# Kernel tuning notes

Measured on AMD Instinct MI355X. Metric: run time of the kernel, lower is better.

Reference implementation:

```python
import jax, jax.numpy as jnp
import numpy as np

N, E, B = 50000, 800000, 512
D_IN = 128
H = [128, 128, 128, 256, 128]
OUT = 2


def setup_inputs() -> dict:
    key = jax.random.key(0)
    ks = jax.random.split(key, 24)

    def w(k, i, o):
        return (jax.random.normal(k, (i, o), jnp.float32) / np.sqrt(i)).astype(jnp.float32)

    x = jax.random.normal(ks[0], (N, D_IN), jnp.float32)
    edge_index = jax.random.randint(ks[1], (2, E), 0, N)
    batch = (jnp.arange(N) * B) // N  # sorted graph ids, every graph non-empty

    return {
        "x": x,
        "edge_index": edge_index,
        "batch": batch,
        # SAGEConv k: out = mean_aggr(x_j) @ Wl + bl + x @ Wr  (PyG default: bias on lin_l, none on lin_r)
        "Wl1": w(ks[2], D_IN, H[0]), "Wr1": w(ks[3], D_IN, H[0]), "bl1": jnp.zeros((H[0],), jnp.float32),
        "Wl2": w(ks[4], H[0], H[1]), "Wr2": w(ks[5], H[0], H[1]), "bl2": jnp.zeros((H[1],), jnp.float32),
        "Wl3": w(ks[6], H[1], H[2]), "Wr3": w(ks[7], H[1], H[2]), "bl3": jnp.zeros((H[2],), jnp.float32),
        "W_f1": w(ks[8], H[2], H[3]), "b_f1": jnp.zeros((H[3],), jnp.float32),
        "W_f2": w(ks[9], H[3], H[4]), "b_f2": jnp.zeros((H[4],), jnp.float32),
        "W_sm": w(ks[10], H[4], OUT), "b_sm": jnp.zeros((OUT,), jnp.float32),
        "W_news": w(ks[11], D_IN, OUT), "b_news": jnp.zeros((OUT,), jnp.float32),
        "W_cat": w(ks[12], 2 * OUT, 1), "b_cat": jnp.zeros((1,), jnp.float32),
    }


def _sage(x, src, dst, Wl, Wr, bl):
    # mean aggregation of source-node features onto destination nodes
    msg = x[src]                                                     # [E, d] gather
    s = jax.ops.segment_sum(msg, dst, num_segments=N)                # [N, d] scatter-add
    cnt = jax.ops.segment_sum(jnp.ones((src.shape[0],), x.dtype), dst, num_segments=N)
    mean = s / jnp.maximum(cnt, 1.0)[:, None]
    return mean @ Wl + bl + x @ Wr


def reference(x, edge_index, batch, Wl1, Wr1, bl1, Wl2, Wr2, bl2, Wl3, Wr3, bl3,
              W_f1, b_f1, W_f2, b_f2, W_sm, b_sm, W_news, b_news, W_cat, b_cat):
    src, dst = edge_index[0], edge_index[1]
    h = jax.nn.relu(_sage(x, src, dst, Wl1, Wr1, bl1))
    h = jax.nn.relu(_sage(h, src, dst, Wl2, Wr2, bl2))
    h = jax.nn.relu(_sage(h, src, dst, Wl3, Wr3, bl3))

    h = jax.ops.segment_max(h, batch, num_segments=B)                # global_max_pool -> [B, H2]
    h = jax.nn.relu(h @ W_f1 + b_f1)
    h = jax.nn.relu(h @ W_f2 + b_f2)
    h = jax.nn.relu(h @ W_sm + b_sm)                                 # [B, OUT]

    # root = first node index of each graph (batch is sorted)
    root = jax.ops.segment_min(jnp.arange(N), batch, num_segments=B)  # [B]
    news = jax.nn.relu(x[root] @ W_news + b_news)                    # [B, OUT]

    out = jnp.concatenate([h, news], axis=-1) @ W_cat + b_cat        # [B, 1]
    return jax.nn.sigmoid(out)
```

## Files before the change

kernel.cpp:

```cpp
#include <hip/hip_runtime.h>
#include <hip/hip_bf16.h>
#include <math.h>

#define D 128
#define SA 144

typedef __attribute__((ext_vector_type(8))) short bf16x8;
typedef __attribute__((ext_vector_type(4))) float f32x4;

static __device__ __forceinline__ short f2b(float f) {
    unsigned u = __builtin_bit_cast(unsigned, f);
    unsigned r = (u + 0x7FFFu + ((u >> 16) & 1u)) >> 16;
    return (short)r;
}
static __device__ __forceinline__ float b2f(short b) {
    unsigned u = ((unsigned)(unsigned short)b) << 16;
    return __builtin_bit_cast(float, u);
}


__global__ __launch_bounds__(256) void conv_x_kernel(const float* __restrict__ x,
                                                     short* __restrict__ xb, int total4) {
    int idx = blockIdx.x * 256 + threadIdx.x;
    if (idx >= total4) return;
    float4 v = ((const float4*)x)[idx];
    short4 o;
    o.x = f2b(v.x); o.y = f2b(v.y); o.z = f2b(v.z); o.w = f2b(v.w);
    ((short4*)xb)[idx] = o;
}

struct WPack { const float* w[6]; short* o[6]; };
__global__ __launch_bounds__(256) void conv_w_kernel(WPack p) {
    const float* W = p.w[blockIdx.y];
    short* O = p.o[blockIdx.y];
    int idx = blockIdx.x * 256 + threadIdx.x;
    int k = idx >> 7, nn = idx & 127;
    O[nn * D + k] = f2b(W[k * D + nn]);
}


__global__ void deg_kernel(const int* __restrict__ dst, int* __restrict__ deg, int E) {
    int e = blockIdx.x * blockDim.x + threadIdx.x;
    if (e < E) atomicAdd(&deg[dst[e]], 1);
}

__global__ __launch_bounds__(256) void block_sum_kernel(const int* __restrict__ deg,
                                                        int* __restrict__ bsum, int n) {
    __shared__ int red[256];
    int b = blockIdx.x, tid = threadIdx.x;
    int base = b * 1024 + tid * 4;
    int s = 0;
    if (base + 3 < n) {
        int4 v = *(const int4*)(deg + base);
        s = v.x + v.y + v.z + v.w;
    } else {
        for (int i = 0; i < 4; ++i) if (base + i < n) s += deg[base + i];
    }
    red[tid] = s;
    __syncthreads();
    for (int off = 128; off; off >>= 1) {
        if (tid < off) red[tid] += red[tid + off];
        __syncthreads();
    }
    if (tid == 0) bsum[b] = red[0];
}

__global__ void bsum_scan_kernel(int* __restrict__ bsum, int nb) {
    int lane = threadIdx.x;
    int v = (lane < nb) ? bsum[lane] : 0;
    for (int off = 1; off < 64; off <<= 1) {
        int t = __shfl_up(v, off, 64);
        if (lane >= off) v += t;
    }
    int ex = __shfl_up(v, 1, 64);
    if (lane == 0) ex = 0;
    if (lane < nb) bsum[lane] = ex;
}

__global__ __launch_bounds__(256) void emit_kernel(const int* __restrict__ deg,
                                                   const int* __restrict__ boff,
                                                   int* __restrict__ row_ptr,
                                                   float* __restrict__ inv_deg,
                                                   int* __restrict__ gcursor,
                                                   int n, int E) {
    __shared__ int tsum[256];
    int b = blockIdx.x, tid = threadIdx.x;
    int base = b * 1024 + tid * 4;
    int v[4]; int s = 0;
#pragma unroll
    for (int i = 0; i < 4; ++i) {
        int idx = base + i;
        v[i] = (idx < n) ? deg[idx] : 0;
        s += v[i];
    }
    tsum[tid] = s;
    __syncthreads();
    for (int off = 1; off < 256; off <<= 1) {
        int t = (tid >= off) ? tsum[tid - off] : 0;
        __syncthreads();
        tsum[tid] += t;
        __syncthreads();
    }
    int run = boff[b] + tsum[tid] - s;
#pragma unroll
    for (int i = 0; i < 4; ++i) {
        int idx = base + i;
        if (idx < n) {
            row_ptr[idx] = run;
            inv_deg[idx] = 1.0f / (float)((v[i] > 0) ? v[i] : 1);
            if ((idx & 127) == 0) gcursor[idx >> 7] = run;
            run += v[i];
        }
    }
    if (b == 0 && tid == 0) row_ptr[n] = E;
}


#define EPB 4096
__global__ __launch_bounds__(256) void bin_kernel(const int* __restrict__ src,
                                                  const int* __restrict__ dst,
                                                  int* __restrict__ gcursor,
                                                  int2* __restrict__ binned, int E) {
    __shared__ int hist[512];
    __shared__ int base[512];
    int tid = threadIdx.x;
    int e0 = blockIdx.x * EPB;
    hist[tid] = 0; hist[tid + 256] = 0;
    __syncthreads();
    int sv[16], dv[16], bv[16];
#pragma unroll
    for (int i = 0; i < 16; ++i) {
        int e = e0 + i * 256 + tid;
        if (e < E) {
            sv[i] = src[e]; dv[i] = dst[e];
            bv[i] = dv[i] >> 7;
            atomicAdd(&hist[bv[i]], 1);
        } else bv[i] = -1;
    }
    __syncthreads();
    {
        int c0 = hist[tid];
        base[tid] = c0 ? atomicAdd(&gcursor[tid], c0) : 0;
        hist[tid] = 0;
        int c1 = hist[tid + 256];
        base[tid + 256] = c1 ? atomicAdd(&gcursor[tid + 256], c1) : 0;
        hist[tid + 256] = 0;
    }
    __syncthreads();
#pragma unroll
    for (int i = 0; i < 16; ++i) {
        if (bv[i] >= 0) {
            int off = atomicAdd(&hist[bv[i]], 1);
            binned[base[bv[i]] + off] = make_int2(sv[i], dv[i]);
        }
    }
}

__global__ __launch_bounds__(256) void place_kernel(const int2* __restrict__ binned,
                                                    const int* __restrict__ row_ptr,
                                                    int* __restrict__ col, int n) {
    __shared__ int cur[128];
    int b = blockIdx.x, tid = threadIdx.x;
    int node0 = b << 7;
    if (tid < 128) {
        int nd = node0 + tid;
        cur[tid] = (nd < n) ? row_ptr[nd] : 0;
    }
    int node1 = node0 + 128; if (node1 > n) node1 = n;
    int start = row_ptr[node0];
    int end   = row_ptr[node1];
    __syncthreads();
    for (int i = start + tid; i < end; i += 256) {
        int2 e = binned[i];
        int pos = atomicAdd(&cur[e.y & 127], 1);
        col[pos] = e.x;
    }
}


__global__ void agg_kernel(const short* __restrict__ h, const int* __restrict__ row_ptr,
                           const int* __restrict__ col, const float* __restrict__ inv_deg,
                           short* __restrict__ out, int n) {
    int w = (blockIdx.x * blockDim.x + threadIdx.x) >> 6;
    int lane = threadIdx.x & 63;
    if (w >= n) return;
    int s = row_ptr[w], e = row_ptr[w + 1];
    int g = lane >> 4, l16 = lane & 15;
    float acc[8];
#pragma unroll
    for (int q = 0; q < 8; ++q) acc[q] = 0.f;
    for (int p = s + g; p < e; p += 4) {
        int j = col[p];
        bf16x8 v = *(const bf16x8*)(h + (size_t)j * D + l16 * 8);
#pragma unroll
        for (int q = 0; q < 8; ++q) acc[q] += b2f(v[q]);
    }
#pragma unroll
    for (int q = 0; q < 8; ++q) {
        acc[q] += __shfl_xor(acc[q], 16, 64);
        acc[q] += __shfl_xor(acc[q], 32, 64);
    }
    if (g == 0) {
        float sc = inv_deg[w];
        bf16x8 o;
#pragma unroll
        for (int q = 0; q < 8; ++q) o[q] = f2b(acc[q] * sc);
        *(bf16x8*)(out + (size_t)w * D + l16 * 8) = o;
    }
}


__global__ __launch_bounds__(256) void sage_mm_mfma(
        const short* __restrict__ Aagg, const short* __restrict__ Hin,
        const short* __restrict__ WlT,  const short* __restrict__ WrT,
        const float* __restrict__ bl,   short* __restrict__ out, int M) {
    __shared__ short lA[128 * SA];
    __shared__ short lW[128 * SA];
    int tid  = threadIdx.x;
    int wave = tid >> 6, lane = tid & 63;
    int row0 = blockIdx.x * 128;
    int mrow = wave * 32;
    int m16  = lane & 15, quad = lane >> 4;

    f32x4 acc[2][8];
#pragma unroll
    for (int i = 0; i < 2; ++i)
#pragma unroll
        for (int j = 0; j < 8; ++j) acc[i][j] = (f32x4){0.f, 0.f, 0.f, 0.f};

#pragma unroll
    for (int half = 0; half < 2; ++half) {
        const short* A = half ? Hin : Aagg;
        const short* W = half ? WrT : WlT;
#pragma unroll
        for (int it = 0; it < 8; ++it) {
            int idx = it * 256 + tid;
            int r = idx >> 4, c8 = (idx & 15) << 3;
            bf16x8 va = {0, 0, 0, 0, 0, 0, 0, 0};
            int gr = row0 + r;
            if (gr < M) va = *(const bf16x8*)(A + (size_t)gr * D + c8);
            *(bf16x8*)(&lA[r * SA + c8]) = va;
            bf16x8 vw = *(const bf16x8*)(W + r * D + c8);
            *(bf16x8*)(&lW[r * SA + c8]) = vw;
        }
        __syncthreads();
#pragma unroll
        for (int ks = 0; ks < 4; ++ks) {
            int kb = ks * 32 + quad * 8;
            bf16x8 a0 = *(const bf16x8*)(&lA[(mrow +      m16) * SA + kb]);
            bf16x8 a1 = *(const bf16x8*)(&lA[(mrow + 16 + m16) * SA + kb]);
#pragma unroll
            for (int nt = 0; nt < 8; ++nt) {
                bf16x8 b = *(const bf16x8*)(&lW[(nt * 16 + m16) * SA + kb]);
                acc[0][nt] = __builtin_amdgcn_mfma_f32_16x16x32_bf16(a0, b, acc[0][nt], 0, 0, 0);
                acc[1][nt] = __builtin_amdgcn_mfma_f32_16x16x32_bf16(a1, b, acc[1][nt], 0, 0, 0);
            }
        }
        __syncthreads();
    }
#pragma unroll
    for (int mt = 0; mt < 2; ++mt) {
#pragma unroll
        for (int r = 0; r < 4; ++r) {
            int grow = row0 + mrow + mt * 16 + quad * 4 + r;
            if (grow < M) {
#pragma unroll
                for (int nt = 0; nt < 8; ++nt) {
                    int gcol = nt * 16 + m16;
                    float v = acc[mt][nt][r] + bl[gcol];
                    out[(size_t)grow * D + gcol] = f2b(fmaxf(v, 0.f));
                }
            }
        }
    }
}


__global__ void pool_kernel(const short* __restrict__ h, const int* __restrict__ batch,
                            float* __restrict__ pooled, int* __restrict__ root, int n) {
    int g = blockIdx.x;
    int f = threadIdx.x;
    int lo = 0, hi = n;
    while (lo < hi) { int m = (lo + hi) >> 1; if (batch[m] < g) lo = m + 1; else hi = m; }
    int start = lo;
    hi = n;
    while (lo < hi) { int m = (lo + hi) >> 1; if (batch[m] < g + 1) lo = m + 1; else hi = m; }
    int end = lo;
    if (f == 0) root[g] = start;
    float m = -3.4e38f;
    for (int i = start; i < end; ++i) m = fmaxf(m, b2f(h[(size_t)i * D + f]));
    pooled[(size_t)g * D + f] = m;
}


__global__ __launch_bounds__(256) void head_kernel(
        const float* __restrict__ pooled, const int* __restrict__ root,
        const float* __restrict__ x,
        const float* __restrict__ W_f1, const float* __restrict__ b_f1,
        const float* __restrict__ W_f2, const float* __restrict__ b_f2,
        const float* __restrict__ W_sm, const float* __restrict__ b_sm,
        const float* __restrict__ W_news, const float* __restrict__ b_news,
        const float* __restrict__ W_cat, const float* __restrict__ b_cat,
        float* __restrict__ out) {
    int g = blockIdx.x;
    int tid = threadIdx.x;
    __shared__ float p[128], t1[256], t2[128], hs[2], nw[2];
    if (tid < 128) p[tid] = pooled[(size_t)g * D + tid];
    __syncthreads();
    float a1 = b_f1[tid];
    for (int k = 0; k < 128; ++k) a1 += p[k] * W_f1[k * 256 + tid];
    t1[tid] = fmaxf(a1, 0.f);
    __syncthreads();
    if (tid < 128) {
        float a2 = b_f2[tid];
        for (int k = 0; k < 256; ++k) a2 += t1[k] * W_f2[k * 128 + tid];
        t2[tid] = fmaxf(a2, 0.f);
    }
    __syncthreads();
    if (tid < 2) {
        float a3 = b_sm[tid];
        for (int k = 0; k < 128; ++k) a3 += t2[k] * W_sm[k * 2 + tid];
        hs[tid] = fmaxf(a3, 0.f);
        const float* xr = x + (size_t)root[g] * D;
        float a4 = b_news[tid];
        for (int k = 0; k < 128; ++k) a4 += xr[k] * W_news[k * 2 + tid];
        nw[tid] = fmaxf(a4, 0.f);
    }
    __syncthreads();
    if (tid == 0) {
        float o = b_cat[0] + hs[0] * W_cat[0] + hs[1] * W_cat[1]
                           + nw[0] * W_cat[2] + nw[1] * W_cat[3];
        out[g] = 1.0f / (1.0f + __expf(-o));
    }
}


extern "C" void kernel_launch(void* const* d_in, const int* in_sizes, int n_in,
                              void* d_out, int out_size, void* d_ws, size_t ws_size,
                              hipStream_t stream) {
    const float* x      = (const float*)d_in[0];
    const int*   edge   = (const int*)d_in[1];
    const int*   batch  = (const int*)d_in[2];
    const float* Wl1 = (const float*)d_in[3];
    const float* Wr1 = (const float*)d_in[4];
    const float* bl1 = (const float*)d_in[5];
    const float* Wl2 = (const float*)d_in[6];
    const float* Wr2 = (const float*)d_in[7];
    const float* bl2 = (const float*)d_in[8];
    const float* Wl3 = (const float*)d_in[9];
    const float* Wr3 = (const float*)d_in[10];
    const float* bl3 = (const float*)d_in[11];
    const float* W_f1 = (const float*)d_in[12];
    const float* b_f1 = (const float*)d_in[13];
    const float* W_f2 = (const float*)d_in[14];
    const float* b_f2 = (const float*)d_in[15];
    const float* W_sm = (const float*)d_in[16];
    const float* b_sm = (const float*)d_in[17];
    const float* W_news = (const float*)d_in[18];
    const float* b_news = (const float*)d_in[19];
    const float* W_cat = (const float*)d_in[20];
    const float* b_cat = (const float*)d_in[21];
    float* out = (float*)d_out;

    const int E = in_sizes[1] / 2;
    const int n = in_sizes[2];
    const int B = out_size;

    const int* src = edge;
    const int* dst = edge + E;

    char* ws = (char*)d_ws;
    size_t off = 0;
    auto carve = [&](size_t bytes) {
        void* pt = ws + off;
        off = (off + bytes + 255) & ~(size_t)255;
        return pt;
    };
    int*   deg     = (int*)carve((size_t)n * 4);
    int*   row_ptr = (int*)carve((size_t)(n + 1) * 4);
    float* inv_deg = (float*)carve((size_t)n * 4);
    int*   col     = (int*)carve((size_t)E * 4);
    int*   bsum    = (int*)carve((size_t)256 * 4);
    int*   gcursor = (int*)carve((size_t)512 * 4);
    int2*  binned  = (int2*)carve((size_t)E * 8);
    short* xb      = (short*)carve((size_t)n * D * 2);
    short* aggb    = (short*)carve((size_t)n * D * 2);
    short* hA      = (short*)carve((size_t)n * D * 2);
    short* hB      = (short*)carve((size_t)n * D * 2);
    short* Wt[6];
    for (int i = 0; i < 6; ++i) Wt[i] = (short*)carve((size_t)D * D * 2);
    float* pooled  = (float*)carve((size_t)B * D * 4);
    int*   root    = (int*)carve((size_t)B * 4);
    (void)ws_size;

    int total4 = n * D / 4;
    conv_x_kernel<<<(total4 + 255) / 256, 256, 0, stream>>>(x, xb, total4);
    WPack wp;
    wp.w[0] = Wl1; wp.w[1] = Wr1; wp.w[2] = Wl2; wp.w[3] = Wr2; wp.w[4] = Wl3; wp.w[5] = Wr3;
    for (int i = 0; i < 6; ++i) wp.o[i] = Wt[i];
    conv_w_kernel<<<dim3(64, 6), 256, 0, stream>>>(wp);

    int nb = (n + 1023) / 1024;
    int NB = (n + 127) / 128;
    hipMemsetAsync(deg, 0, (size_t)n * 4, stream);
    deg_kernel<<<(E + 255) / 256, 256, 0, stream>>>(dst, deg, E);
    block_sum_kernel<<<nb, 256, 0, stream>>>(deg, bsum, n);
    bsum_scan_kernel<<<1, 64, 0, stream>>>(bsum, nb);
    emit_kernel<<<nb, 256, 0, stream>>>(deg, bsum, row_ptr, inv_deg, gcursor, n, E);
    bin_kernel<<<(E + EPB - 1) / EPB, 256, 0, stream>>>(src, dst, gcursor, binned, E);
    place_kernel<<<NB, 256, 0, stream>>>(binned, row_ptr, col, n);

    int agg_blocks = (n * 64 + 255) / 256;
    int mm_blocks  = (n + 127) / 128;

    agg_kernel<<<agg_blocks, 256, 0, stream>>>(xb, row_ptr, col, inv_deg, aggb, n);
    sage_mm_mfma<<<mm_blocks, 256, 0, stream>>>(aggb, xb, Wt[0], Wt[1], bl1, hA, n);
    agg_kernel<<<agg_blocks, 256, 0, stream>>>(hA, row_ptr, col, inv_deg, aggb, n);
    sage_mm_mfma<<<mm_blocks, 256, 0, stream>>>(aggb, hA, Wt[2], Wt[3], bl2, hB, n);
    agg_kernel<<<agg_blocks, 256, 0, stream>>>(hB, row_ptr, col, inv_deg, aggb, n);
    sage_mm_mfma<<<mm_blocks, 256, 0, stream>>>(aggb, hB, Wt[4], Wt[5], bl3, hA, n);

    pool_kernel<<<B, 128, 0, stream>>>(hA, batch, pooled, root, n);
    head_kernel<<<B, 256, 0, stream>>>(pooled, root, x,
                                       W_f1, b_f1, W_f2, b_f2, W_sm, b_sm,
                                       W_news, b_news, W_cat, b_cat, out);
}
```

Baseline: 373.0 us.

## Fuse preprocessing and pool/head kernels, rebuild CSR from bucket histograms

Merges the x and weight bf16 conversions with a per-bucket destination histogram into one prep kernel. The per-node degree atomics and three-kernel scan are replaced by a 512-entry bucket scan, with per-node degrees and row pointers now computed inside place_kernel. The aggregation loop is unrolled by two to keep more gathers in flight, and pool and head are fused into a single kernel. The goal is fewer launches and fewer global atomics, at the cost of an extra pass over binned edges in place_kernel.

```diff
diff --git a/kernel.cpp b/kernel.cpp
--- a/kernel.cpp
+++ b/kernel.cpp
@@ -19,100 +19,73 @@
 }
 
 
-__global__ __launch_bounds__(256) void conv_x_kernel(const float* __restrict__ x,
-                                                     short* __restrict__ xb, int total4) {
-    int idx = blockIdx.x * 256 + threadIdx.x;
-    if (idx >= total4) return;
-    float4 v = ((const float4*)x)[idx];
-    short4 o;
-    o.x = f2b(v.x); o.y = f2b(v.y); o.z = f2b(v.z); o.w = f2b(v.w);
-    ((short4*)xb)[idx] = o;
-}
-
-struct WPack { const float* w[6]; short* o[6]; };
-__global__ __launch_bounds__(256) void conv_w_kernel(WPack p) {
-    const float* W = p.w[blockIdx.y];
-    short* O = p.o[blockIdx.y];
-    int idx = blockIdx.x * 256 + threadIdx.x;
-    int k = idx >> 7, nn = idx & 127;
-    O[nn * D + k] = f2b(W[k * D + nn]);
-}
-
-
-__global__ void deg_kernel(const int* __restrict__ dst, int* __restrict__ deg, int E) {
-    int e = blockIdx.x * blockDim.x + threadIdx.x;
-    if (e < E) atomicAdd(&deg[dst[e]], 1);
-}
-
-__global__ __launch_bounds__(256) void block_sum_kernel(const int* __restrict__ deg,
-                                                        int* __restrict__ bsum, int n) {
-    __shared__ int red[256];
-    int b = blockIdx.x, tid = threadIdx.x;
-    int base = b * 1024 + tid * 4;
-    int s = 0;
-    if (base + 3 < n) {
-        int4 v = *(const int4*)(deg + base);
-        s = v.x + v.y + v.z + v.w;
-    } else {
-        for (int i = 0; i < 4; ++i) if (base + i < n) s += deg[base + i];
-    }
-    red[tid] = s;
-    __syncthreads();
-    for (int off = 128; off; off >>= 1) {
-        if (tid < off) red[tid] += red[tid + off];
-        __syncthreads();
-    }
-    if (tid == 0) bsum[b] = red[0];
-}
-
-__global__ void bsum_scan_kernel(int* __restrict__ bsum, int nb) {
-    int lane = threadIdx.x;
-    int v = (lane < nb) ? bsum[lane] : 0;
-    for (int off = 1; off < 64; off <<= 1) {
-        int t = __shfl_up(v, off, 64);
-        if (lane >= off) v += t;
-    }
-    int ex = __shfl_up(v, 1, 64);
-    if (lane == 0) ex = 0;
-    if (lane < nb) bsum[lane] = ex;
-}
-
-__global__ __launch_bounds__(256) void emit_kernel(const int* __restrict__ deg,
-                                                   const int* __restrict__ boff,
-                                                   int* __restrict__ row_ptr,
-                                                   float* __restrict__ inv_deg,
-                                                   int* __restrict__ gcursor,
-                                                   int n, int E) {
-    __shared__ int tsum[256];
-    int b = blockIdx.x, tid = threadIdx.x;
-    int base = b * 1024 + tid * 4;
-    int v[4]; int s = 0;
-#pragma unroll
-    for (int i = 0; i < 4; ++i) {
-        int idx = base + i;
-        v[i] = (idx < n) ? deg[idx] : 0;
-        s += v[i];
-    }
-    tsum[tid] = s;
+struct PrepArgs {
+    const float* x; short* xb; int total4; int xb_blocks;
+    const float* w[6]; short* wo[6]; int w_blocks;
+    const int* dst; int* bcnt; int E;
+};
+
+__global__ __launch_bounds__(256) void prep_kernel(PrepArgs a) {
+    int bid = blockIdx.x, tid = threadIdx.x;
+    if (bid < a.xb_blocks) {
+        int idx = bid * 256 + tid;
+        if (idx < a.total4) {
+            float4 v = ((const float4*)a.x)[idx];
+            short4 o;
+            o.x = f2b(v.x); o.y = f2b(v.y); o.z = f2b(v.z); o.w = f2b(v.w);
+            ((short4*)a.xb)[idx] = o;
+        }
+        return;
+    }
+    if (bid < a.xb_blocks + a.w_blocks) {
+        int idx4 = (bid - a.xb_blocks) * 256 + tid;
+        int base = idx4 * 4;
+        int m = base >> 14;
+        int i = base & 16383;
+        const float* W = a.w[m];
+        short* O = a.wo[m];
+        int k = i >> 7, nn = i & 127;
+        float4 v = *(const float4*)(W + k * D + nn);
+        O[(nn + 0) * D + k] = f2b(v.x);
+        O[(nn + 1) * D + k] = f2b(v.y);
+        O[(nn + 2) * D + k] = f2b(v.z);
+        O[(nn + 3) * D + k] = f2b(v.w);
+        return;
+    }
+    __shared__ int hist[512];
+    hist[tid] = 0; hist[tid + 256] = 0;
+    __syncthreads();
+    int e0 = (bid - a.xb_blocks - a.w_blocks) * 4096;
+#pragma unroll
+    for (int i = 0; i < 16; ++i) {
+        int e = e0 + i * 256 + tid;
+        if (e < a.E) atomicAdd(&hist[a.dst[e] >> 7], 1);
+    }
+    __syncthreads();
+    int c = hist[tid];       if (c) atomicAdd(&a.bcnt[tid], c);
+    c = hist[tid + 256];     if (c) atomicAdd(&a.bcnt[tid + 256], c);
+}
+
+
+__global__ __launch_bounds__(256) void scan512_kernel(const int* __restrict__ bcnt,
+                                                      int* __restrict__ gbase,
+                                                      int* __restrict__ gcursor) {
+    __shared__ int sc[256];
+    int tid = threadIdx.x;
+    int a0 = bcnt[2 * tid], a1 = bcnt[2 * tid + 1];
+    int s = a0 + a1;
+    sc[tid] = s;
     __syncthreads();
     for (int off = 1; off < 256; off <<= 1) {
-        int t = (tid >= off) ? tsum[tid - off] : 0;
-        __syncthreads();
-        tsum[tid] += t;
-        __syncthreads();
-    }
-    int run = boff[b] + tsum[tid] - s;
-#pragma unroll
-    for (int i = 0; i < 4; ++i) {
-        int idx = base + i;
-        if (idx < n) {
-            row_ptr[idx] = run;
-            inv_deg[idx] = 1.0f / (float)((v[i] > 0) ? v[i] : 1);
-            if ((idx & 127) == 0) gcursor[idx >> 7] = run;
-            run += v[i];
-        }
-    }
-    if (b == 0 && tid == 0) row_ptr[n] = E;
+        int t = (tid >= off) ? sc[tid - off] : 0;
+        __syncthreads();
+        sc[tid] += t;
+        __syncthreads();
+    }
+    int ex = sc[tid] - s;
+    gbase[2 * tid] = ex;         gcursor[2 * tid] = ex;
+    gbase[2 * tid + 1] = ex + a0; gcursor[2 * tid + 1] = ex + a0;
+    if (tid == 255) gbase[512] = sc[255];
 }
 
 
@@ -156,19 +129,44 @@
     }
 }
 
+
 __global__ __launch_bounds__(256) void place_kernel(const int2* __restrict__ binned,
-                                                    const int* __restrict__ row_ptr,
-                                                    int* __restrict__ col, int n) {
+                                                    const int* __restrict__ gbase,
+                                                    int* __restrict__ row_ptr,
+                                                    float* __restrict__ inv_deg,
+                                                    int* __restrict__ col,
+                                                    int n, int E, int NB) {
+    __shared__ int cnt[128];
+    __shared__ int sc[128];
     __shared__ int cur[128];
     int b = blockIdx.x, tid = threadIdx.x;
     int node0 = b << 7;
+    int node1 = node0 + 128; if (node1 > n) node1 = n;
+    int start = gbase[b], end = gbase[b + 1];
+    if (tid < 128) cnt[tid] = 0;
+    __syncthreads();
+    for (int i = start + tid; i < end; i += 256)
+        atomicAdd(&cnt[binned[i].y & 127], 1);
+    __syncthreads();
+    if (tid < 128) sc[tid] = cnt[tid];
+    __syncthreads();
+    for (int off = 1; off < 128; off <<= 1) {
+        int t = (tid < 128 && tid >= off) ? sc[tid - off] : 0;
+        __syncthreads();
+        if (tid < 128) sc[tid] += t;
+        __syncthreads();
+    }
     if (tid < 128) {
         int nd = node0 + tid;
-        cur[tid] = (nd < n) ? row_ptr[nd] : 0;
-    }
-    int node1 = node0 + 128; if (node1 > n) node1 = n;
-    int start = row_ptr[node0];
-    int end   = row_ptr[node1];
+        if (nd < node1) {
+            int c = cnt[tid];
+            int base = start + sc[tid] - c;
+            row_ptr[nd] = base;
+            inv_deg[nd] = 1.0f / (float)((c > 0) ? c : 1);
+            cur[tid] = base;
+        }
+    }
+    if (b == NB - 1 && tid == 0) row_ptr[n] = E;
     __syncthreads();
     for (int i = start + tid; i < end; i += 256) {
         int2 e = binned[i];
@@ -189,7 +187,18 @@
     float acc[8];
 #pragma unroll
     for (int q = 0; q < 8; ++q) acc[q] = 0.f;
-    for (int p = s + g; p < e; p += 4) {
+    int p = s + g;
+    for (; p + 4 < e; p += 8) {
+        int j0 = col[p];
+        int j1 = col[p + 4];
+        bf16x8 v0 = *(const bf16x8*)(h + (size_t)j0 * D + l16 * 8);
+        bf16x8 v1 = *(const bf16x8*)(h + (size_t)j1 * D + l16 * 8);
+#pragma unroll
+        for (int q = 0; q < 8; ++q) acc[q] += b2f(v0[q]);
+#pragma unroll
+        for (int q = 0; q < 8; ++q) acc[q] += b2f(v1[q]);
+    }
+    if (p < e) {
         int j = col[p];
         bf16x8 v = *(const bf16x8*)(h + (size_t)j * D + l16 * 8);
 #pragma unroll
@@ -276,36 +285,31 @@
 }
 
 
-__global__ void pool_kernel(const short* __restrict__ h, const int* __restrict__ batch,
-                            float* __restrict__ pooled, int* __restrict__ root, int n) {
+__global__ __launch_bounds__(256) void poolhead_kernel(
+        const short* __restrict__ h, const int* __restrict__ batch,
+        const float* __restrict__ x,
+        const float* __restrict__ W_f1, const float* __restrict__ b_f1,
+        const float* __restrict__ W_f2, const float* __restrict__ b_f2,
+        const float* __restrict__ W_sm, const float* __restrict__ b_sm,
+        const float* __restrict__ W_news, const float* __restrict__ b_news,
+        const float* __restrict__ W_cat, const float* __restrict__ b_cat,
+        float* __restrict__ out, int n) {
     int g = blockIdx.x;
-    int f = threadIdx.x;
+    int tid = threadIdx.x;
+    int f = tid & 127, half = tid >> 7;
+    __shared__ float pm[256];
+    __shared__ float p[128], t1[256], t2[128], hs[2], nw[2];
     int lo = 0, hi = n;
     while (lo < hi) { int m = (lo + hi) >> 1; if (batch[m] < g) lo = m + 1; else hi = m; }
     int start = lo;
     hi = n;
     while (lo < hi) { int m = (lo + hi) >> 1; if (batch[m] < g + 1) lo = m + 1; else hi = m; }
     int end = lo;
-    if (f == 0) root[g] = start;
     float m = -3.4e38f;
-    for (int i = start; i < end; ++i) m = fmaxf(m, b2f(h[(size_t)i * D + f]));
-    pooled[(size_t)g * D + f] = m;
-}
-
-
-__global__ __launch_bounds__(256) void head_kernel(
-        const float* __restrict__ pooled, const int* __restrict__ root,
-        const float* __restrict__ x,
-        const float* __restrict__ W_f1, const float* __restrict__ b_f1,
-        const float* __restrict__ W_f2, const float* __restrict__ b_f2,
-        const float* __restrict__ W_sm, const float* __restrict__ b_sm,
-        const float* __restrict__ W_news, const float* __restrict__ b_news,
-        const float* __restrict__ W_cat, const float* __restrict__ b_cat,
-        float* __restrict__ out) {
-    int g = blockIdx.x;
-    int tid = threadIdx.x;
-    __shared__ float p[128], t1[256], t2[128], hs[2], nw[2];
-    if (tid < 128) p[tid] = pooled[(size_t)g * D + tid];
+    for (int i = start + half; i < end; i += 2) m = fmaxf(m, b2f(h[(size_t)i * D + f]));
+    pm[tid] = m;
+    __syncthreads();
+    if (tid < 128) p[tid] = fmaxf(pm[tid], pm[tid + 128]);
     __syncthreads();
     float a1 = b_f1[tid];
     for (int k = 0; k < 128; ++k) a1 += p[k] * W_f1[k * 256 + tid];
@@ -321,7 +325,7 @@
         float a3 = b_sm[tid];
         for (int k = 0; k < 128; ++k) a3 += t2[k] * W_sm[k * 2 + tid];
         hs[tid] = fmaxf(a3, 0.f);
-        const float* xr = x + (size_t)root[g] * D;
+        const float* xr = x + (size_t)start * D;
         float a4 = b_news[tid];
         for (int k = 0; k < 128; ++k) a4 += xr[k] * W_news[k * 2 + tid];
         nw[tid] = fmaxf(a4, 0.f);
@@ -376,11 +380,11 @@
         off = (off + bytes + 255) & ~(size_t)255;
         return pt;
     };
-    int*   deg     = (int*)carve((size_t)n * 4);
     int*   row_ptr = (int*)carve((size_t)(n + 1) * 4);
     float* inv_deg = (float*)carve((size_t)n * 4);
     int*   col     = (int*)carve((size_t)E * 4);
-    int*   bsum    = (int*)carve((size_t)256 * 4);
+    int*   bcnt    = (int*)carve((size_t)512 * 4);
+    int*   gbase   = (int*)carve((size_t)513 * 4);
     int*   gcursor = (int*)carve((size_t)512 * 4);
     int2*  binned  = (int2*)carve((size_t)E * 8);
     short* xb      = (short*)carve((size_t)n * D * 2);
@@ -389,26 +393,23 @@
     short* hB      = (short*)carve((size_t)n * D * 2);
     short* Wt[6];
     for (int i = 0; i < 6; ++i) Wt[i] = (short*)carve((size_t)D * D * 2);
-    float* pooled  = (float*)carve((size_t)B * D * 4);
-    int*   root    = (int*)carve((size_t)B * 4);
     (void)ws_size;
 
-    int total4 = n * D / 4;
-    conv_x_kernel<<<(total4 + 255) / 256, 256, 0, stream>>>(x, xb, total4);
-    WPack wp;
-    wp.w[0] = Wl1; wp.w[1] = Wr1; wp.w[2] = Wl2; wp.w[3] = Wr2; wp.w[4] = Wl3; wp.w[5] = Wr3;
-    for (int i = 0; i < 6; ++i) wp.o[i] = Wt[i];
-    conv_w_kernel<<<dim3(64, 6), 256, 0, stream>>>(wp);
-
-    int nb = (n + 1023) / 1024;
+    hipMemsetAsync(bcnt, 0, 512 * 4, stream);
+    PrepArgs pa;
+    pa.x = x; pa.xb = xb; pa.total4 = n * D / 4;
+    pa.xb_blocks = (pa.total4 + 255) / 256;
+    pa.w[0] = Wl1; pa.w[1] = Wr1; pa.w[2] = Wl2; pa.w[3] = Wr2; pa.w[4] = Wl3; pa.w[5] = Wr3;
+    for (int i = 0; i < 6; ++i) pa.wo[i] = Wt[i];
+    pa.w_blocks = (6 * D * D) / 1024;
+    pa.dst = dst; pa.bcnt = bcnt; pa.E = E;
+    int h_blocks = (E + 4095) / 4096;
+    prep_kernel<<<pa.xb_blocks + pa.w_blocks + h_blocks, 256, 0, stream>>>(pa);
+
     int NB = (n + 127) / 128;
-    hipMemsetAsync(deg, 0, (size_t)n * 4, stream);
-    deg_kernel<<<(E + 255) / 256, 256, 0, stream>>>(dst, deg, E);
-    block_sum_kernel<<<nb, 256, 0, stream>>>(deg, bsum, n);
-    bsum_scan_kernel<<<1, 64, 0, stream>>>(bsum, nb);
-    emit_kernel<<<nb, 256, 0, stream>>>(deg, bsum, row_ptr, inv_deg, gcursor, n, E);
+    scan512_kernel<<<1, 256, 0, stream>>>(bcnt, gbase, gcursor);
     bin_kernel<<<(E + EPB - 1) / EPB, 256, 0, stream>>>(src, dst, gcursor, binned, E);
-    place_kernel<<<NB, 256, 0, stream>>>(binned, row_ptr, col, n);
+    place_kernel<<<NB, 256, 0, stream>>>(binned, gbase, row_ptr, inv_deg, col, n, E, NB);
 
     int agg_blocks = (n * 64 + 255) / 256;
     int mm_blocks  = (n + 127) / 128;
@@ -420,8 +421,7 @@
     agg_kernel<<<agg_blocks, 256, 0, stream>>>(hB, row_ptr, col, inv_deg, aggb, n);
     sage_mm_mfma<<<mm_blocks, 256, 0, stream>>>(aggb, hB, Wt[4], Wt[5], bl3, hA, n);
 
-    pool_kernel<<<B, 128, 0, stream>>>(hA, batch, pooled, root, n);
-    head_kernel<<<B, 256, 0, stream>>>(pooled, root, x,
-                                       W_f1, b_f1, W_f2, b_f2, W_sm, b_sm,
-                                       W_news, b_news, W_cat, b_cat, out);
-}
+    poolhead_kernel<<<B, 256, 0, stream>>>(hA, batch, x,
+                                           W_f1, b_f1, W_f2, b_f2, W_sm, b_sm,
+                                           W_news, b_news, W_cat, b_cat, out, n);
+}
```

Measured after the change: 316.2 us. 1.18x faster.
